# Kernel optimization log

Measured on AMD Instinct MI355X. Metric: run time of the kernel, lower is better.

The kernel has to match this reference:

```python
import jax, jax.numpy as jnp
import numpy as np

DIM = 1024
HEADS = 16
DIM_HEAD = 64
NUM_FREQS = 16
INNER = HEADS * DIM_HEAD


def rotate_half(x):
    # matches torch: cat((-x[..., 1::2], x[..., ::2]), dim=-1)
    x1 = x[..., ::2]
    x2 = x[..., 1::2]
    return jnp.concatenate((-x2, x1), axis=-1)


def rope_fourier_cache(seq_len, head_dim, num_freqs):
    freqs = 10000.0 ** (-jnp.arange(0, head_dim, 2, dtype=jnp.float32) / head_dim)  # [hd/2]
    pos = jnp.arange(seq_len, dtype=jnp.float32)[:, None]  # [n,1]
    angles = pos * freqs  # [n, hd/2]
    sin = jnp.sin(angles)
    cos = jnp.cos(angles)
    # interleave-duplicate each value per pair: [n, hd]
    sin = jnp.stack([sin, sin], axis=-1).reshape(seq_len, head_dim)
    cos = jnp.stack([cos, cos], axis=-1).reshape(seq_len, head_dim)
    ffreqs = jnp.arange(1, num_freqs + 1, dtype=jnp.float32)  # [F]
    p = jnp.arange(seq_len, dtype=jnp.float32)[:, None]  # [n,1]
    fourier = jnp.concatenate([jnp.sin(p * ffreqs), jnp.cos(p * ffreqs)], axis=-1)  # [n, 2F]
    return sin, cos, fourier


def setup_inputs() -> dict:
    key = jax.random.key(0)
    ks = jax.random.split(key, 6)
    b, n = 4, 2048
    x = jax.random.normal(ks[0], (b, n, DIM), dtype=jnp.float32)
    w_qkv = jax.random.normal(ks[1], (3 * INNER, DIM), dtype=jnp.float32) * (DIM ** -0.5)
    w_fproj = jax.random.normal(ks[2], (DIM_HEAD, 2 * NUM_FREQS), dtype=jnp.float32) * ((2 * NUM_FREQS) ** -0.5)
    b_fproj = jax.random.normal(ks[3], (DIM_HEAD,), dtype=jnp.float32) * 0.02
    w_out = jax.random.normal(ks[4], (DIM, INNER), dtype=jnp.float32) * (INNER ** -0.5)
    b_out = jax.random.normal(ks[5], (DIM,), dtype=jnp.float32) * 0.02
    return {"x": x, "w_qkv": w_qkv, "w_fproj": w_fproj, "b_fproj": b_fproj,
            "w_out": w_out, "b_out": b_out}


def reference(x, w_qkv, w_fproj, b_fproj, w_out, b_out):
    b, n, _ = x.shape
    scale = DIM_HEAD ** -0.5
    qkv = x @ w_qkv.T  # [b, n, 3*inner]
    q, k, v = jnp.split(qkv, 3, axis=-1)
    def to_heads(t):
        return t.reshape(b, n, HEADS, DIM_HEAD).transpose(0, 2, 1, 3)  # [b,h,n,d]
    q, k, v = to_heads(q), to_heads(k), to_heads(v)
    sin, cos, fourier = rope_fourier_cache(n, DIM_HEAD, NUM_FREQS)
    fenc = fourier @ w_fproj.T + b_fproj  # [n, d]
    fenc = fenc[None, None]  # [1,1,n,d]
    q = q * cos + rotate_half(q) * sin + fenc
    k = k * cos + rotate_half(k) * sin + fenc
    dots = jnp.einsum('bhid,bhjd->bhij', q, k) * scale
    attn = jax.nn.softmax(dots, axis=-1)
    out = jnp.einsum('bhij,bhjd->bhid', attn, v)
    out = out.transpose(0, 2, 1, 3).reshape(b, n, INNER)
    return out @ w_out.T + b_out
```

## Files before the change

### kernel.cpp

```cpp
#include <hip/hip_runtime.h>
#include <math.h>

#define NB 4
#define SEQ 2048
#define DIMM 1024
#define NH 16
#define DHD 64
#define NFQ 16

typedef __bf16 bf16x8 __attribute__((ext_vector_type(8)));
typedef __bf16 bf16x4 __attribute__((ext_vector_type(4)));
typedef float f32x4 __attribute__((ext_vector_type(4)));

#if __has_builtin(__builtin_amdgcn_exp2f)
#define EXP2F(x) __builtin_amdgcn_exp2f(x)
#else
#define EXP2F(x) exp2f(x)
#endif

__device__ inline unsigned short f2bf(float f) {
  unsigned int u = __builtin_bit_cast(unsigned int, f);
  u += 0x7fffu + ((u >> 16) & 1u);
  return (unsigned short)(u >> 16);
}

#define GLL16(gp, lp) __builtin_amdgcn_global_load_lds( \
    (__attribute__((address_space(1))) void*)(gp), \
    (__attribute__((address_space(3))) void*)(lp), 16, 0, 0)

__global__ __launch_bounds__(64) void rope_tab_kernel(const float* __restrict__ w_fproj,
                                                      const float* __restrict__ b_fproj,
                                                      float4* __restrict__ tab) {
  const int pos = blockIdx.x;
  const int d = threadIdx.x;
  __shared__ float four[2 * NFQ];
  if (d < NFQ) {
    double a = (double)pos * (double)(d + 1);
    four[d] = (float)sin(a);
    four[d + NFQ] = (float)cos(a);
  }
  __syncthreads();
  float fe = b_fproj[d];
  const float* wr = w_fproj + d * 2 * NFQ;
#pragma unroll
  for (int j = 0; j < 2 * NFQ; ++j) fe += four[j] * wr[j];
  const int i = d >> 1;
  const double freq = exp(((double)(-2 * i)) / 64.0 * log(10000.0));
  const float angle = (float)pos * (float)freq;
  const float c = (float)cos((double)angle);
  const float s = (float)sin((double)angle);
  tab[(pos << 6) + d] = make_float4(c, s, fe, 0.f);
}

__global__ __launch_bounds__(256) void f2bf_kernel(const float* __restrict__ src,
                                                   unsigned short* __restrict__ dst, int n4) {
  for (int i = blockIdx.x * 256 + threadIdx.x; i < n4; i += gridDim.x * 256) {
    const float4 v = ((const float4*)src)[i];
    ushort4 o;
    o.x = f2bf(v.x); o.y = f2bf(v.y); o.z = f2bf(v.z); o.w = f2bf(v.w);
    ((ushort4*)dst)[i] = o;
  }
}

template<int EPI>
__global__ __launch_bounds__(256) void gemm_bt(const unsigned short* __restrict__ A,
                                               const unsigned short* __restrict__ Bw,
                                               int K,
                                               float* __restrict__ outF,
                                               unsigned short* __restrict__ outQ,
                                               unsigned short* __restrict__ outK,
                                               unsigned short* __restrict__ outV,
                                               const float4* __restrict__ tab,
                                               const float* __restrict__ bias,
                                               float qscale) {
  __shared__ __align__(16) unsigned short As[2][128 * 32];
  __shared__ __align__(16) unsigned short Bs[2][128 * 32];
  const int t = threadIdx.x, l = t & 63, w = t >> 6;
  const int wr = w >> 1, wc = w & 1;
  const int nwg = gridDim.x * gridDim.y;
  int flat = blockIdx.x + gridDim.x * blockIdx.y;
  flat = (flat & 7) * (nwg >> 3) + (flat >> 3);
  const int bm = (flat / gridDim.x) * 128, bn = (flat % gridDim.x) * 128;
  const f32x4 z = {0.f, 0.f, 0.f, 0.f};
  f32x4 acc[4][4];
#pragma unroll
  for (int m = 0; m < 4; ++m)
#pragma unroll
    for (int n = 0; n < 4; ++n) acc[m][n] = z;

  auto stage = [&](int k0, int buf) {
#pragma unroll
    for (int j = 0; j < 2; ++j) {
      const int Bb = w * 2048 + j * 1024 + l * 16;
      const int row = Bb >> 6, bin = Bb & 63;
      const int sb = bin ^ ((row & 3) << 4);
      GLL16(A  + (size_t)(bm + row) * K + k0 + (sb >> 1), (char*)(&As[buf][0]) + w * 2048 + j * 1024);
      GLL16(Bw + (size_t)(bn + row) * K + k0 + (sb >> 1), (char*)(&Bs[buf][0]) + w * 2048 + j * 1024);
    }
  };

  stage(0, 0);
  int cur = 0;
  for (int k0 = 0; k0 < K; k0 += 32) {
    __syncthreads();
    if (k0 + 32 < K) stage(k0 + 32, cur ^ 1);

    bf16x8 af[4], bfr[4];
#pragma unroll
    for (int m = 0; m < 4; ++m) {
      const int row = wr * 64 + m * 16 + (l & 15);
      const int bin = ((l >> 4) * 16) ^ ((row & 3) << 4);
      af[m] = *(const bf16x8*)((const char*)(&As[cur][0]) + row * 64 + bin);
    }
#pragma unroll
    for (int n = 0; n < 4; ++n) {
      const int row = wc * 64 + n * 16 + (l & 15);
      const int bin = ((l >> 4) * 16) ^ ((row & 3) << 4);
      bfr[n] = *(const bf16x8*)((const char*)(&Bs[cur][0]) + row * 64 + bin);
    }
#pragma unroll
    for (int m = 0; m < 4; ++m)
#pragma unroll
      for (int n = 0; n < 4; ++n)
        acc[m][n] = __builtin_amdgcn_mfma_f32_16x16x32_bf16(af[m], bfr[n], acc[m][n], 0, 0, 0);
    cur ^= 1;
  }

  const int c = l & 15;
  if (EPI == 0) {
    const int which = bn >> 10;
    const int h = ((bn & 1023) >> 6) + wc;
    if (which == 2) {
#pragma unroll
      for (int m = 0; m < 4; ++m)
#pragma unroll
        for (int n = 0; n < 4; ++n) {
          const int d = n * 16 + c;
#pragma unroll
          for (int r = 0; r < 4; ++r) {
            const int mrow = bm + wr * 64 + m * 16 + (l >> 4) * 4 + r;
            const int b = mrow >> 11, pos = mrow & (SEQ - 1);
            outV[((size_t)(b * NH + h) * DHD + d) * SEQ + pos] = f2bf(acc[m][n][r]);
          }
        }
    } else {
      unsigned short* dst = (which == 0) ? outQ : outK;
      const float sc = (which == 0) ? qscale : 1.f;
      const int laneE = (l & 48) | ((2 * c) & 15);
      const int laneO = (l & 48) | ((2 * c + 1) & 15);
      const bool hi = (c >= 8);
#pragma unroll
      for (int m = 0; m < 4; ++m)
#pragma unroll
        for (int r = 0; r < 4; ++r) {
          const int mrow = bm + wr * 64 + m * 16 + (l >> 4) * 4 + r;
          const int b = mrow >> 11, pos = mrow & (SEQ - 1);
          const float V0 = acc[m][0][r], V1 = acc[m][1][r];
          const float V2 = acc[m][2][r], V3 = acc[m][3][r];
          const float e0 = __shfl(V0, laneE), e1 = __shfl(V1, laneE);
          const float e2 = __shfl(V2, laneE), e3 = __shfl(V3, laneE);
          const float o0 = __shfl(V0, laneO), o1 = __shfl(V1, laneO);
          const float o2 = __shfl(V2, laneO), o3 = __shfl(V3, laneO);
          const float rot0 = -(hi ? o1 : o0);
          const float rot1 = -(hi ? o3 : o2);
          const float rot2 =  (hi ? e1 : e0);
          const float rot3 =  (hi ? e3 : e2);
          const float4 t0 = tab[(pos << 6) + c];
          const float4 t1 = tab[(pos << 6) + 16 + c];
          const float4 t2 = tab[(pos << 6) + 32 + c];
          const float4 t3 = tab[(pos << 6) + 48 + c];
          unsigned short* drow = dst + ((size_t)(b * NH + h) * SEQ + pos) * DHD + c;
          drow[0]  = f2bf((V0 * t0.x + rot0 * t0.y + t0.z) * sc);
          drow[16] = f2bf((V1 * t1.x + rot1 * t1.y + t1.z) * sc);
          drow[32] = f2bf((V2 * t2.x + rot2 * t2.y + t2.z) * sc);
          drow[48] = f2bf((V3 * t3.x + rot3 * t3.y + t3.z) * sc);
        }
    }
  } else {
#pragma unroll
    for (int m = 0; m < 4; ++m)
#pragma unroll
      for (int n = 0; n < 4; ++n) {
        const int ncol = bn + wc * 64 + n * 16 + c;
        const float bb = bias[ncol];
#pragma unroll
        for (int r = 0; r < 4; ++r) {
          const int mrow = bm + wr * 64 + m * 16 + (l >> 4) * 4 + r;
          outF[(size_t)mrow * DIMM + ncol] = acc[m][n][r] + bb;
        }
      }
  }
}

__global__ __launch_bounds__(256, 3) void attn_kernel(const unsigned short* __restrict__ qbf,
                                                      const unsigned short* __restrict__ kbf,
                                                      const unsigned short* __restrict__ vt,
                                                      unsigned short* __restrict__ ao) {
  __shared__ __align__(16) unsigned short Ks[2][64 * 64], Vts[2][64 * 64];
  __shared__ __align__(16) unsigned short Ps[4][32 * 64];
  const int t = threadIdx.x, l = t & 63, w = t >> 6, g = l >> 4, q = l & 15;
  int flat = blockIdx.x + (blockIdx.y << 4);
  flat = (flat & 7) * 128 + (flat >> 3);
  const int q0 = (flat & 15) * 128;
  const int bh = flat >> 4;
  const int b = bh >> 4, h = bh & 15;
  const size_t hbase = (size_t)bh * SEQ * DHD;
  const f32x4 z = {0.f, 0.f, 0.f, 0.f};
  const int swz = (q & 7) << 4;
  const int woff = w * 32;

  bf16x8 ones;
#pragma unroll
  for (int j = 0; j < 8; ++j) ones[j] = (__bf16)1.0f;

  auto stageKV = [&](int kt, int buf) {
#pragma unroll
    for (int j = 0; j < 2; ++j) {
      const int base = (w * 2 + j) * 1024;
      const int row = (base + l * 16) >> 7;
      const int sb = ((l & 7) * 16) ^ ((row & 7) << 4);
      GLL16(kbf + hbase + (size_t)(kt + row) * DHD + (sb >> 1), (char*)(&Ks[buf][0]) + base);
      GLL16(vt  + hbase + (size_t)row * SEQ + kt + (sb >> 1),  (char*)(&Vts[buf][0]) + base);
    }
  };

  bf16x8 qf[2][2];
#pragma unroll
  for (int qb = 0; qb < 2; ++qb)
#pragma unroll
    for (int ks = 0; ks < 2; ++ks)
      qf[qb][ks] = *(const bf16x8*)(qbf + hbase +
          (size_t)(q0 + woff + qb * 16 + q) * DHD + ks * 32 + g * 8);

  stageKV(0, 0);

  f32x4 of[2][4], lsum[2];
#pragma unroll
  for (int qb = 0; qb < 2; ++qb) {
    lsum[qb] = z;
#pragma unroll
    for (int nd = 0; nd < 4; ++nd) of[qb][nd] = z;
  }

  int cur = 0;
  for (int kt = 0; kt < SEQ; kt += 64) {
    __syncthreads();
    if (kt + 64 < SEQ) stageKV(kt + 64, cur ^ 1);

    const char* Kc = (const char*)(&Ks[cur][0]);
    const char* Vc = (const char*)(&Vts[cur][0]);

    f32x4 sf[2][4];
#pragma unroll
    for (int qb = 0; qb < 2; ++qb)
#pragma unroll
      for (int n = 0; n < 4; ++n) sf[qb][n] = z;
#pragma unroll
    for (int ks = 0; ks < 2; ++ks) {
      bf16x8 kf[4];
#pragma unroll
      for (int n = 0; n < 4; ++n)
        kf[n] = *(const bf16x8*)(Kc + (n * 16 + q) * 128 + ((ks * 64 + g * 16) ^ swz));
      __builtin_amdgcn_s_setprio(1);
#pragma unroll
      for (int qb = 0; qb < 2; ++qb)
#pragma unroll
        for (int n = 0; n < 4; ++n)
          sf[qb][n] = __builtin_amdgcn_mfma_f32_16x16x32_bf16(kf[n], qf[qb][ks], sf[qb][n], 0, 0, 0);
      __builtin_amdgcn_s_setprio(0);
    }

#pragma unroll
    for (int qb = 0; qb < 2; ++qb) {
      char* prow = (char*)(&Ps[w][0]) + (qb * 16 + q) * 128;
#pragma unroll
      for (int n = 0; n < 4; ++n) {
        bf16x4 pk;
        pk[0] = (__bf16)EXP2F(sf[qb][n][0]);
        pk[1] = (__bf16)EXP2F(sf[qb][n][1]);
        pk[2] = (__bf16)EXP2F(sf[qb][n][2]);
        pk[3] = (__bf16)EXP2F(sf[qb][n][3]);
        *(bf16x4*)(prow + ((n * 32 + g * 8) ^ swz)) = pk;
      }
    }

    bf16x8 vf[4][2];
#pragma unroll
    for (int nd = 0; nd < 4; ++nd)
#pragma unroll
      for (int ks = 0; ks < 2; ++ks)
        vf[nd][ks] = *(const bf16x8*)(Vc + (nd * 16 + q) * 128 + ((ks * 64 + g * 16) ^ swz));

#pragma unroll
    for (int qb = 0; qb < 2; ++qb) {
      const char* prow = (const char*)(&Ps[w][0]) + (qb * 16 + q) * 128;
      bf16x8 pa[2];
#pragma unroll
      for (int ks = 0; ks < 2; ++ks)
        pa[ks] = *(const bf16x8*)(prow + ((ks * 64 + g * 16) ^ swz));
      __builtin_amdgcn_s_setprio(1);
#pragma unroll
      for (int ks = 0; ks < 2; ++ks)
        lsum[qb] = __builtin_amdgcn_mfma_f32_16x16x32_bf16(pa[ks], ones, lsum[qb], 0, 0, 0);
#pragma unroll
      for (int nd = 0; nd < 4; ++nd)
#pragma unroll
        for (int ks = 0; ks < 2; ++ks)
          of[qb][nd] = __builtin_amdgcn_mfma_f32_16x16x32_bf16(pa[ks], vf[nd][ks], of[qb][nd], 0, 0, 0);
      __builtin_amdgcn_s_setprio(0);
    }
    cur ^= 1;
  }

#pragma unroll
  for (int qb = 0; qb < 2; ++qb)
#pragma unroll
    for (int r = 0; r < 4; ++r) {
      const float ir = 1.f / lsum[qb][r];
      const int pos = q0 + woff + qb * 16 + g * 4 + r;
#pragma unroll
      for (int nd = 0; nd < 4; ++nd) {
        const int col = h * DHD + nd * 16 + q;
        ao[((size_t)(b * SEQ + pos)) * DIMM + col] = f2bf(of[qb][nd][r] * ir);
      }
    }
}

extern "C" void kernel_launch(void* const* d_in, const int* in_sizes, int n_in,
                              void* d_out, int out_size, void* d_ws, size_t ws_size,
                              hipStream_t stream) {
  const float* x       = (const float*)d_in[0];
  const float* w_qkv   = (const float*)d_in[1];
  const float* w_fproj = (const float*)d_in[2];
  const float* b_fproj = (const float*)d_in[3];
  const float* w_out   = (const float*)d_in[4];
  const float* b_out   = (const float*)d_in[5];
  char* ws = (char*)d_ws;

  unsigned short* qbf    = (unsigned short*)(ws);
  unsigned short* kbf    = (unsigned short*)(ws + 16777216);
  unsigned short* vt     = (unsigned short*)(ws + 33554432);
  unsigned short* xbf    = (unsigned short*)(ws + 50331648);
  unsigned short* aobf   = (unsigned short*)(ws + 67108864);
  unsigned short* wqkvbf = (unsigned short*)(ws + 83886080);
  unsigned short* woutbf = (unsigned short*)(ws + 90177536);
  float4*         tab    = (float4*)(ws + 92274688);

  const float kLog2e = 1.4426950408889634f;

  hipLaunchKernelGGL(rope_tab_kernel, dim3(SEQ), dim3(DHD), 0, stream, w_fproj, b_fproj, tab);
  hipLaunchKernelGGL(f2bf_kernel, dim3(2048), dim3(256), 0, stream, x, xbf, (NB*SEQ*DIMM)/4);
  hipLaunchKernelGGL(f2bf_kernel, dim3(768), dim3(256), 0, stream, w_qkv, wqkvbf, (3*DIMM*DIMM)/4);
  hipLaunchKernelGGL(f2bf_kernel, dim3(256), dim3(256), 0, stream, w_out, woutbf, (DIMM*DIMM)/4);
  hipLaunchKernelGGL((gemm_bt<0>), dim3(24, 64), dim3(256), 0, stream,
                     xbf, wqkvbf, DIMM, (float*)nullptr, qbf, kbf, vt, tab,
                     (const float*)nullptr, 0.125f * kLog2e);
  hipLaunchKernelGGL(attn_kernel, dim3(SEQ/128, NB*NH), dim3(256), 0, stream, qbf, kbf, vt, aobf);
  hipLaunchKernelGGL((gemm_bt<1>), dim3(8, 64), dim3(256), 0, stream,
                     aobf, woutbf, DIMM, (float*)d_out, (unsigned short*)nullptr,
                     (unsigned short*)nullptr, (unsigned short*)nullptr, (const float4*)nullptr,
                     b_out, 1.0f);
}
```

Baseline: 209.8 us.

## Single-buffer attention K/V tiles for higher occupancy; regroup GEMM tile mapping per XCD

The attention kernel drops double-buffered K/V shared memory in favour of a single buffer with a barrier before and after each load, and raises the launch-bounds occupancy hint from 3 to 5 workgroups. The aim is to hide load latency by running more resident waves rather than by software prefetch. The GEMM block-to-tile mapping now assigns each XCD a contiguous band of 8 M-tiles and groups blocks in 8x4 tiles along N, for better L2 locality. The risks are exposed load latency from the extra barrier each iteration and possible register spilling under the tighter occupancy bound.

```diff
diff --git a/kernel.cpp b/kernel.cpp
--- a/kernel.cpp
+++ b/kernel.cpp
@@ -77,10 +77,11 @@
   __shared__ __align__(16) unsigned short Bs[2][128 * 32];
   const int t = threadIdx.x, l = t & 63, w = t >> 6;
   const int wr = w >> 1, wc = w & 1;
-  const int nwg = gridDim.x * gridDim.y;
-  int flat = blockIdx.x + gridDim.x * blockIdx.y;
-  flat = (flat & 7) * (nwg >> 3) + (flat >> 3);
-  const int bm = (flat / gridDim.x) * 128, bn = (flat % gridDim.x) * 128;
+  const int orig = blockIdx.x + gridDim.x * blockIdx.y;
+  const int xcd = orig & 7, idx = orig >> 3;
+  const int sc = idx >> 5, r5 = idx & 31;
+  const int bm = ((xcd << 3) + (r5 >> 2)) * 128;
+  const int bn = ((sc << 2) + (r5 & 3)) * 128;
   const f32x4 z = {0.f, 0.f, 0.f, 0.f};
   f32x4 acc[4][4];
 #pragma unroll
@@ -145,7 +146,7 @@
         }
     } else {
       unsigned short* dst = (which == 0) ? outQ : outK;
-      const float sc = (which == 0) ? qscale : 1.f;
+      const float sc2 = (which == 0) ? qscale : 1.f;
       const int laneE = (l & 48) | ((2 * c) & 15);
       const int laneO = (l & 48) | ((2 * c + 1) & 15);
       const bool hi = (c >= 8);
@@ -170,10 +171,10 @@
           const float4 t2 = tab[(pos << 6) + 32 + c];
           const float4 t3 = tab[(pos << 6) + 48 + c];
           unsigned short* drow = dst + ((size_t)(b * NH + h) * SEQ + pos) * DHD + c;
-          drow[0]  = f2bf((V0 * t0.x + rot0 * t0.y + t0.z) * sc);
-          drow[16] = f2bf((V1 * t1.x + rot1 * t1.y + t1.z) * sc);
-          drow[32] = f2bf((V2 * t2.x + rot2 * t2.y + t2.z) * sc);
-          drow[48] = f2bf((V3 * t3.x + rot3 * t3.y + t3.z) * sc);
+          drow[0]  = f2bf((V0 * t0.x + rot0 * t0.y + t0.z) * sc2);
+          drow[16] = f2bf((V1 * t1.x + rot1 * t1.y + t1.z) * sc2);
+          drow[32] = f2bf((V2 * t2.x + rot2 * t2.y + t2.z) * sc2);
+          drow[48] = f2bf((V3 * t3.x + rot3 * t3.y + t3.z) * sc2);
         }
     }
   } else {
@@ -192,11 +193,11 @@
   }
 }
 
-__global__ __launch_bounds__(256, 3) void attn_kernel(const unsigned short* __restrict__ qbf,
+__global__ __launch_bounds__(256, 5) void attn_kernel(const unsigned short* __restrict__ qbf,
                                                       const unsigned short* __restrict__ kbf,
                                                       const unsigned short* __restrict__ vt,
                                                       unsigned short* __restrict__ ao) {
-  __shared__ __align__(16) unsigned short Ks[2][64 * 64], Vts[2][64 * 64];
+  __shared__ __align__(16) unsigned short Ks[64 * 64], Vts[64 * 64];
   __shared__ __align__(16) unsigned short Ps[4][32 * 64];
   const int t = threadIdx.x, l = t & 63, w = t >> 6, g = l >> 4, q = l & 15;
   int flat = blockIdx.x + (blockIdx.y << 4);
@@ -213,14 +214,14 @@
 #pragma unroll
   for (int j = 0; j < 8; ++j) ones[j] = (__bf16)1.0f;
 
-  auto stageKV = [&](int kt, int buf) {
+  auto stageKV = [&](int kt) {
 #pragma unroll
     for (int j = 0; j < 2; ++j) {
       const int base = (w * 2 + j) * 1024;
       const int row = (base + l * 16) >> 7;
       const int sb = ((l & 7) * 16) ^ ((row & 7) << 4);
-      GLL16(kbf + hbase + (size_t)(kt + row) * DHD + (sb >> 1), (char*)(&Ks[buf][0]) + base);
-      GLL16(vt  + hbase + (size_t)row * SEQ + kt + (sb >> 1),  (char*)(&Vts[buf][0]) + base);
+      GLL16(kbf + hbase + (size_t)(kt + row) * DHD + (sb >> 1), (char*)Ks + base);
+      GLL16(vt  + hbase + (size_t)row * SEQ + kt + (sb >> 1),  (char*)Vts + base);
     }
   };
 
@@ -232,8 +233,6 @@
       qf[qb][ks] = *(const bf16x8*)(qbf + hbase +
           (size_t)(q0 + woff + qb * 16 + q) * DHD + ks * 32 + g * 8);
 
-  stageKV(0, 0);
-
   f32x4 of[2][4], lsum[2];
 #pragma unroll
   for (int qb = 0; qb < 2; ++qb) {
@@ -242,13 +241,10 @@
     for (int nd = 0; nd < 4; ++nd) of[qb][nd] = z;
   }
 
-  int cur = 0;
   for (int kt = 0; kt < SEQ; kt += 64) {
     __syncthreads();
-    if (kt + 64 < SEQ) stageKV(kt + 64, cur ^ 1);
-
-    const char* Kc = (const char*)(&Ks[cur][0]);
-    const char* Vc = (const char*)(&Vts[cur][0]);
+    stageKV(kt);
+    __syncthreads();
 
     f32x4 sf[2][4];
 #pragma unroll
@@ -260,7 +256,7 @@
       bf16x8 kf[4];
 #pragma unroll
       for (int n = 0; n < 4; ++n)
-        kf[n] = *(const bf16x8*)(Kc + (n * 16 + q) * 128 + ((ks * 64 + g * 16) ^ swz));
+        kf[n] = *(const bf16x8*)((const char*)Ks + (n * 16 + q) * 128 + ((ks * 64 + g * 16) ^ swz));
       __builtin_amdgcn_s_setprio(1);
 #pragma unroll
       for (int qb = 0; qb < 2; ++qb)
@@ -289,7 +285,7 @@
     for (int nd = 0; nd < 4; ++nd)
 #pragma unroll
       for (int ks = 0; ks < 2; ++ks)
-        vf[nd][ks] = *(const bf16x8*)(Vc + (nd * 16 + q) * 128 + ((ks * 64 + g * 16) ^ swz));
+        vf[nd][ks] = *(const bf16x8*)((const char*)Vts + (nd * 16 + q) * 128 + ((ks * 64 + g * 16) ^ swz));
 
 #pragma unroll
     for (int qb = 0; qb < 2; ++qb) {
@@ -309,7 +305,6 @@
           of[qb][nd] = __builtin_amdgcn_mfma_f32_16x16x32_bf16(pa[ks], vf[nd][ks], of[qb][nd], 0, 0, 0);
       __builtin_amdgcn_s_setprio(0);
     }
-    cur ^= 1;
   }
 
 #pragma unroll
```

Measured after the change: 372.7 us. 1.78x slower.
